# Optimization experiments

Hardware: AMD Instinct MI355X
Metric: run time of the kernel (lower is better)

Reference implementation:

```python
import jax, jax.numpy as jnp
import numpy as np

B, C, L = 4, 256, 4096
H = 8
DK = C // H


def setup_inputs() -> dict:
    key = jax.random.key(0)
    kx, kq, kk, kv, kl = jax.random.split(key, 5)
    scale = 1.0 / np.sqrt(C)
    return {
        "x": jax.random.normal(kx, (B, C, L), dtype=jnp.float32),
        "Wq": jax.random.normal(kq, (C, C), dtype=jnp.float32) * scale,
        "Wk": jax.random.normal(kk, (C, C), dtype=jnp.float32) * scale,
        "Wv": jax.random.normal(kv, (C, C), dtype=jnp.float32) * scale,
        "Wl": jax.random.normal(kl, (C, C), dtype=jnp.float32) * scale,
    }


def reference(x, Wq, Wk, Wv, Wl):
    # Conv1d with kernel_size=1, no bias == channel-mixing matmul per position.
    def proj(W, t):  # W: [C_out, C_in], t: [B, C_in, L] -> [B, L, H, DK]
        y = jnp.einsum('oc,bcl->blo', W, t)
        return y.reshape(B, L, H, DK)

    q = proj(Wq, x)  # [B, L, H, DK]
    k = proj(Wk, x)
    v = proj(Wv, x)

    # scores: [B, H, L, L]
    scores = jnp.einsum('bqhd,bkhd->bhqk', q, k) / jnp.sqrt(jnp.float32(DK))
    p_attn = jax.nn.softmax(scores, axis=-1)
    # attention output with post-ReLU: [B, L, H, DK] -> [B, L, C]
    out = jax.nn.relu(jnp.einsum('bhqk,bkhd->bqhd', p_attn, v)).reshape(B, L, C)
    # last_conv: [B, C_out, L]
    return jnp.einsum('oc,blc->bol', Wl, out)
```

## Files before the change

kernel.cpp:

```cpp
#include <hip/hip_runtime.h>

#define L_DIM 4096
#define C_DIM 256
#define B_DIM 4
#define NH 8
#define DK 32

#define QSCALE 0.25507694f

typedef __bf16 bf16x8 __attribute__((ext_vector_type(8)));
typedef float  f32x4  __attribute__((ext_vector_type(4)));
typedef float  f32x8  __attribute__((ext_vector_type(8)));
typedef float  f32x16 __attribute__((ext_vector_type(16)));

static __device__ __forceinline__ unsigned pk_bf16(float lo, float hi) {
    unsigned a = __builtin_bit_cast(unsigned, lo) + 0x8000u;
    unsigned b = __builtin_bit_cast(unsigned, hi) + 0x8000u;
    return __builtin_amdgcn_perm(b, a, 0x07060302u);
}

__global__ __launch_bounds__(256) void transpose_x_kernel(
    const float* __restrict__ x, __bf16* __restrict__ xt)
{
    const int t  = threadIdx.x;
    const int l0 = blockIdx.x * 64;
    const int c0 = blockIdx.y * 64;
    const int b  = blockIdx.z;

    __shared__ __attribute__((aligned(16))) float T[64][65];

    {
        const int r  = t >> 2;
        const int lc = (t & 3) * 16;
        const float* xp = x + ((size_t)b * C_DIM + c0 + r) * L_DIM + l0 + lc;
        #pragma unroll
        for (int k = 0; k < 4; ++k)
            *(f32x4*)&T[r][lc + k * 4] = *(const f32x4*)(xp + k * 4);
    }
    __syncthreads();
    {
        const int l  = t >> 2;
        const int cc = (t & 3) * 16;
        unsigned u[8];
        #pragma unroll
        for (int i = 0; i < 8; ++i)
            u[i] = pk_bf16(T[cc + 2 * i][l], T[cc + 2 * i + 1][l]);
        __bf16* op = xt + ((size_t)b * L_DIM + l0 + l) * C_DIM + c0 + cc;
        *(uint4*)op       = make_uint4(u[0], u[1], u[2], u[3]);
        *(uint4*)(op + 8) = make_uint4(u[4], u[5], u[6], u[7]);
    }
}

__global__ __launch_bounds__(256) void proj_mfma_kernel(
    const __bf16* __restrict__ xt, const float* __restrict__ Wq,
    const float* __restrict__ Wk, const float* __restrict__ Wv,
    __bf16* __restrict__ Qb, __bf16* __restrict__ Kb, __bf16* __restrict__ Vb)
{
    const int t    = threadIdx.x;
    const int wave = t >> 6;
    const int lane = t & 63;
    const int n32  = lane & 31;
    const int hl   = lane >> 5;
    const int l0   = blockIdx.x * 128;
    const int ob   = blockIdx.y & 1;
    const int p    = blockIdx.y >> 1;
    const int b    = blockIdx.z;
    const float* W = (p == 0) ? Wq : ((p == 1) ? Wk : Wv);
    const float sc = (p == 0) ? QSCALE : 1.0f;

    __shared__ __attribute__((aligned(16))) __bf16 Wt[128][72];
    __shared__ __attribute__((aligned(16))) __bf16 Xs[128][72];

    const int wo  = t >> 1, wcc = (t & 1) * 32;
    const int xl  = t >> 1, xcc = (t & 1) * 32;
    const float*  wg = W + (size_t)(ob * 128 + wo) * C_DIM + wcc;
    const __bf16* xg = xt + ((size_t)b * L_DIM + l0 + xl) * C_DIM + xcc;

    const int moff = (wave & 1) * 64;
    const int noff = (wave >> 1) * 64;

    f32x16 acc[2][2];
    #pragma unroll
    for (int i = 0; i < 2; ++i)
        #pragma unroll
        for (int j = 0; j < 2; ++j)
            #pragma unroll
            for (int r = 0; r < 16; ++r) acc[i][j][r] = 0.f;

    unsigned wpk[16];
    bf16x8   xpr[4];
    #pragma unroll
    for (int k = 0; k < 8; ++k) {
        f32x4 wv = *(const f32x4*)(wg + k * 4);
        wpk[k * 2]     = pk_bf16(wv[0] * sc, wv[1] * sc);
        wpk[k * 2 + 1] = pk_bf16(wv[2] * sc, wv[3] * sc);
    }
    #pragma unroll
    for (int g = 0; g < 4; ++g) xpr[g] = *(const bf16x8*)(xg + g * 8);

    for (int bk = 0; bk < 4; ++bk) {
        __syncthreads();
        #pragma unroll
        for (int g = 0; g < 4; ++g) {
            *(uint4*)&Wt[wo][wcc + g * 8] =
                make_uint4(wpk[g*4], wpk[g*4+1], wpk[g*4+2], wpk[g*4+3]);
            *(bf16x8*)&Xs[xl][xcc + g * 8] = xpr[g];
        }
        if (bk < 3) {
            #pragma unroll
            for (int k = 0; k < 8; ++k) {
                f32x4 wv = *(const f32x4*)(wg + (bk + 1) * 64 + k * 4);
                wpk[k * 2]     = pk_bf16(wv[0] * sc, wv[1] * sc);
                wpk[k * 2 + 1] = pk_bf16(wv[2] * sc, wv[3] * sc);
            }
            #pragma unroll
            for (int g = 0; g < 4; ++g)
                xpr[g] = *(const bf16x8*)(xg + (bk + 1) * 64 + g * 8);
        }
        __syncthreads();

        #pragma unroll
        for (int ks = 0; ks < 4; ++ks) {
            bf16x8 a0 = *(const bf16x8*)&Wt[moff + n32     ][ks * 16 + hl * 8];
            bf16x8 a1 = *(const bf16x8*)&Wt[moff + 32 + n32][ks * 16 + hl * 8];
            bf16x8 b0 = *(const bf16x8*)&Xs[noff + n32     ][ks * 16 + hl * 8];
            bf16x8 b1 = *(const bf16x8*)&Xs[noff + 32 + n32][ks * 16 + hl * 8];
            acc[0][0] = __builtin_amdgcn_mfma_f32_32x32x16_bf16(a0, b0, acc[0][0], 0, 0, 0);
            acc[0][1] = __builtin_amdgcn_mfma_f32_32x32x16_bf16(a0, b1, acc[0][1], 0, 0, 0);
            acc[1][0] = __builtin_amdgcn_mfma_f32_32x32x16_bf16(a1, b0, acc[1][0], 0, 0, 0);
            acc[1][1] = __builtin_amdgcn_mfma_f32_32x32x16_bf16(a1, b1, acc[1][1], 0, 0, 0);
        }
    }

    #pragma unroll
    for (int mt = 0; mt < 2; ++mt) {
        const int o32 = ob * 128 + moff + mt * 32;
        const int h   = o32 >> 5;
        const int bh  = b * NH + h;
        #pragma unroll
        for (int nt = 0; nt < 2; ++nt) {
            const int l = l0 + noff + nt * 32 + n32;
            if (p < 2) {
                __bf16* out = ((p == 0) ? Qb : Kb) + ((size_t)bh * L_DIM + l) * DK;
                #pragma unroll
                for (int g = 0; g < 4; ++g) {
                    unsigned u0 = pk_bf16(acc[mt][nt][g*4],     acc[mt][nt][g*4+1]);
                    unsigned u1 = pk_bf16(acc[mt][nt][g*4+2],   acc[mt][nt][g*4+3]);
                    *(uint2*)(out + 4 * hl + 8 * g) = make_uint2(u0, u1);
                }
            } else {
                #pragma unroll
                for (int r = 0; r < 16; ++r) {
                    const int dk = (r & 3) + 4 * hl + 8 * (r >> 2);
                    Vb[((size_t)bh * DK + dk) * L_DIM + l] = (__bf16)acc[mt][nt][r];
                }
            }
        }
    }
}

__global__ __launch_bounds__(256) void attn_kernel(
    const __bf16* __restrict__ Q, const __bf16* __restrict__ K,
    const __bf16* __restrict__ V, __bf16* __restrict__ Op0,
    __bf16* __restrict__ Op1, float* __restrict__ Ls)
{
    const int tid   = threadIdx.x;
    const int lane  = tid & 63;
    const int n32   = lane & 31;
    const int hl    = lane >> 5;
    const int wave  = tid >> 6;
    const int h     = blockIdx.y;
    const int b     = blockIdx.z >> 1;
    const int khalf = blockIdx.z & 1;
    const int bh    = b * NH + h;
    const int q0    = blockIdx.x * 256 + wave * 64;

    __shared__ __attribute__((aligned(16))) __bf16 Ks[2][128][40];
    __shared__ __attribute__((aligned(16))) __bf16 Vs[2][32][136];

    bf16x8 qf[2][2];
    #pragma unroll
    for (int qt = 0; qt < 2; ++qt) {
        const __bf16* qp = Q + ((size_t)bh * L_DIM + q0 + qt * 32 + n32) * DK;
        qf[qt][0] = *(const bf16x8*)(qp + hl * 8);
        qf[qt][1] = *(const bf16x8*)(qp + 16 + hl * 8);
    }

    f32x16 oacc[2], lacc[2];
    #pragma unroll
    for (int qt = 0; qt < 2; ++qt)
        #pragma unroll
        for (int r = 0; r < 16; ++r) { oacc[qt][r] = 0.f; lacc[qt][r] = 0.f; }

    const f32x16 z16 = {};

    bf16x8 ones;
    #pragma unroll
    for (int j = 0; j < 8; ++j) ones[j] = (__bf16)1.0f;

    const __bf16* kg = K + (size_t)bh * L_DIM * DK + (size_t)khalf * 2048 * DK
                         + (tid >> 1) * DK + (tid & 1) * 16;
    const __bf16* vg = V + ((size_t)bh * DK + (tid >> 3)) * L_DIM
                         + khalf * 2048 + (tid & 7) * 16;
    const int kr = tid >> 1, kc = (tid & 1) * 16;
    const int j16 = (tid & 7) * 16;
    const int vr  = tid >> 3;

    bf16x8 kreg0 = *(const bf16x8*)(kg);
    bf16x8 kreg1 = *(const bf16x8*)(kg + 8);
    bf16x8 vreg0 = *(const bf16x8*)(vg);
    bf16x8 vreg1 = *(const bf16x8*)(vg + 8);
    {
        *(bf16x8*)&Ks[0][kr][kc]     = kreg0;
        *(bf16x8*)&Ks[0][kr][kc + 8] = kreg1;
        union { bf16x8 v; uint2 u2[2]; } v0, v1;
        v0.v = vreg0; v1.v = vreg1;
        *(uint2*)&Vs[0][vr][j16]      = v0.u2[0];
        *(uint2*)&Vs[0][vr][j16 + 8]  = v0.u2[1];
        *(uint2*)&Vs[0][vr][j16 + 4]  = v1.u2[0];
        *(uint2*)&Vs[0][vr][j16 + 12] = v1.u2[1];
    }
    kreg0 = *(const bf16x8*)(kg + (size_t)1 * 128 * DK);
    kreg1 = *(const bf16x8*)(kg + (size_t)1 * 128 * DK + 8);
    vreg0 = *(const bf16x8*)(vg + 128);
    vreg1 = *(const bf16x8*)(vg + 128 + 8);

    #pragma unroll 2
    for (int kt = 0; kt < 16; ++kt) {
        const int cur = kt & 1;
        __syncthreads();

        if (kt < 15) {
            *(bf16x8*)&Ks[cur ^ 1][kr][kc]     = kreg0;
            *(bf16x8*)&Ks[cur ^ 1][kr][kc + 8] = kreg1;
            union { bf16x8 v; uint2 u2[2]; } v0, v1;
            v0.v = vreg0; v1.v = vreg1;
            *(uint2*)&Vs[cur ^ 1][vr][j16]      = v0.u2[0];
            *(uint2*)&Vs[cur ^ 1][vr][j16 + 8]  = v0.u2[1];
            *(uint2*)&Vs[cur ^ 1][vr][j16 + 4]  = v1.u2[0];
            *(uint2*)&Vs[cur ^ 1][vr][j16 + 12] = v1.u2[1];
            const int nkt = (kt + 2) & 15;
            kreg0 = *(const bf16x8*)(kg + (size_t)nkt * 128 * DK);
            kreg1 = *(const bf16x8*)(kg + (size_t)nkt * 128 * DK + 8);
            vreg0 = *(const bf16x8*)(vg + nkt * 128);
            vreg1 = *(const bf16x8*)(vg + nkt * 128 + 8);
        }

        __builtin_amdgcn_s_setprio(1);
        #pragma unroll
        for (int mt = 0; mt < 4; ++mt) {
            bf16x8 kf0 = *(const bf16x8*)&Ks[cur][mt * 32 + n32][hl * 8];
            bf16x8 kf1 = *(const bf16x8*)&Ks[cur][mt * 32 + n32][16 + hl * 8];
            bf16x8 vfA = *(const bf16x8*)&Vs[cur][n32][mt * 32 + hl * 8];
            bf16x8 vfB = *(const bf16x8*)&Vs[cur][n32][mt * 32 + 16 + hl * 8];
            #pragma unroll
            for (int qt = 0; qt < 2; ++qt) {
                f32x16 s = __builtin_amdgcn_mfma_f32_32x32x16_bf16(
                    kf0, qf[qt][0], z16, 0, 0, 0);
                s = __builtin_amdgcn_mfma_f32_32x32x16_bf16(
                    kf1, qf[qt][1], s, 0, 0, 0);

                f32x8 e0, e1;
                #pragma unroll
                for (int r = 0; r < 8; ++r) {
                    e0[r] = __builtin_amdgcn_exp2f(s[r]);
                    e1[r] = __builtin_amdgcn_exp2f(s[8 + r]);
                }
                bf16x8 p0 = __builtin_convertvector(e0, bf16x8);
                bf16x8 p1 = __builtin_convertvector(e1, bf16x8);

                oacc[qt] = __builtin_amdgcn_mfma_f32_32x32x16_bf16(
                    vfA,  p0, oacc[qt], 0, 0, 0);
                lacc[qt] = __builtin_amdgcn_mfma_f32_32x32x16_bf16(
                    ones, p0, lacc[qt], 0, 0, 0);
                oacc[qt] = __builtin_amdgcn_mfma_f32_32x32x16_bf16(
                    vfB,  p1, oacc[qt], 0, 0, 0);
                lacc[qt] = __builtin_amdgcn_mfma_f32_32x32x16_bf16(
                    ones, p1, lacc[qt], 0, 0, 0);
            }
        }
        __builtin_amdgcn_s_setprio(0);
    }

    __bf16* Op = khalf ? Op1 : Op0;
    #pragma unroll
    for (int qt = 0; qt < 2; ++qt) {
        const int l = q0 + qt * 32 + n32;
        __bf16* ap = Op + ((size_t)b * L_DIM + l) * C_DIM + h * 32 + 4 * hl;
        #pragma unroll
        for (int g = 0; g < 4; ++g) {
            *(uint2*)(ap + 8 * g) = make_uint2(
                pk_bf16(oacc[qt][g*4],     oacc[qt][g*4+1]),
                pk_bf16(oacc[qt][g*4+2],   oacc[qt][g*4+3]));
        }
        Ls[((size_t)khalf * B_DIM * NH + bh) * L_DIM + l] = lacc[qt][0];
    }
}

__global__ __launch_bounds__(256) void final_mfma_kernel(
    const __bf16* __restrict__ Op0, const __bf16* __restrict__ Op1,
    const float* __restrict__ Ls, const float* __restrict__ Wl,
    float* __restrict__ y)
{
    const int t    = threadIdx.x;
    const int wave = t >> 6;
    const int lane = t & 63;
    const int n32  = lane & 31;
    const int hl   = lane >> 5;
    const int l0   = blockIdx.x * 64;
    const int ob   = blockIdx.y;
    const int b    = blockIdx.z;

    __shared__ __attribute__((aligned(16))) __bf16 Wt[128][72];
    __shared__ __attribute__((aligned(16))) __bf16 Xs[64][72];

    const int wo  = t >> 1, wcc = (t & 1) * 32;
    const int xl  = t >> 2, xcc = (t & 3) * 16;
    const float* wg = Wl + (size_t)(ob * 128 + wo) * C_DIM + wcc;
    const size_t obase = ((size_t)b * L_DIM + l0 + xl) * C_DIM + xcc;

    float inv[4];
    {
        const int lidx = l0 + xl;
        #pragma unroll
        for (int bk = 0; bk < 4; ++bk) {
            const int hh = (bk * 64 + xcc) >> 5;
            const float l1 = Ls[((size_t)0 * B_DIM * NH + b * NH + hh) * L_DIM + lidx];
            const float l2 = Ls[((size_t)1 * B_DIM * NH + b * NH + hh) * L_DIM + lidx];
            inv[bk] = __builtin_amdgcn_rcpf(l1 + l2);
        }
    }

    const int moff = (wave & 1) * 64;
    const int noff = (wave >> 1) * 32;

    f32x16 acc[2];
    #pragma unroll
    for (int i = 0; i < 2; ++i)
        #pragma unroll
        for (int r = 0; r < 16; ++r) acc[i][r] = 0.f;

    unsigned wpk[16];
    bf16x8   o1r, o2r;
    #pragma unroll
    for (int k = 0; k < 8; ++k) {
        f32x4 wv = *(const f32x4*)(wg + k * 4);
        wpk[k * 2]     = pk_bf16(wv[0], wv[1]);
        wpk[k * 2 + 1] = pk_bf16(wv[2], wv[3]);
    }
    o1r = *(const bf16x8*)(Op0 + obase);
    o2r = *(const bf16x8*)(Op1 + obase);
    bf16x8 o1r2 = *(const bf16x8*)(Op0 + obase + 8);
    bf16x8 o2r2 = *(const bf16x8*)(Op1 + obase + 8);

    for (int bk = 0; bk < 4; ++bk) {
        __syncthreads();
        #pragma unroll
        for (int g = 0; g < 4; ++g)
            *(uint4*)&Wt[wo][wcc + g * 8] =
                make_uint4(wpk[g*4], wpk[g*4+1], wpk[g*4+2], wpk[g*4+3]);
        {
            unsigned u[4];
            #pragma unroll
            for (int i = 0; i < 4; ++i) {
                float v0 = ((float)o1r[2*i]   + (float)o2r[2*i]  ) * inv[bk];
                float v1 = ((float)o1r[2*i+1] + (float)o2r[2*i+1]) * inv[bk];
                v0 = v0 > 0.f ? v0 : 0.f;
                v1 = v1 > 0.f ? v1 : 0.f;
                u[i] = pk_bf16(v0, v1);
            }
            *(uint4*)&Xs[xl][xcc] = make_uint4(u[0], u[1], u[2], u[3]);
            #pragma unroll
            for (int i = 0; i < 4; ++i) {
                float v0 = ((float)o1r2[2*i]   + (float)o2r2[2*i]  ) * inv[bk];
                float v1 = ((float)o1r2[2*i+1] + (float)o2r2[2*i+1]) * inv[bk];
                v0 = v0 > 0.f ? v0 : 0.f;
                v1 = v1 > 0.f ? v1 : 0.f;
                u[i] = pk_bf16(v0, v1);
            }
            *(uint4*)&Xs[xl][xcc + 8] = make_uint4(u[0], u[1], u[2], u[3]);
        }
        if (bk < 3) {
            #pragma unroll
            for (int k = 0; k < 8; ++k) {
                f32x4 wv = *(const f32x4*)(wg + (bk + 1) * 64 + k * 4);
                wpk[k * 2]     = pk_bf16(wv[0], wv[1]);
                wpk[k * 2 + 1] = pk_bf16(wv[2], wv[3]);
            }
            o1r  = *(const bf16x8*)(Op0 + obase + (bk + 1) * 64);
            o2r  = *(const bf16x8*)(Op1 + obase + (bk + 1) * 64);
            o1r2 = *(const bf16x8*)(Op0 + obase + (bk + 1) * 64 + 8);
            o2r2 = *(const bf16x8*)(Op1 + obase + (bk + 1) * 64 + 8);
        }
        __syncthreads();

        #pragma unroll
        for (int ks = 0; ks < 4; ++ks) {
            bf16x8 a0 = *(const bf16x8*)&Wt[moff + n32     ][ks * 16 + hl * 8];
            bf16x8 a1 = *(const bf16x8*)&Wt[moff + 32 + n32][ks * 16 + hl * 8];
            bf16x8 b0 = *(const bf16x8*)&Xs[noff + n32     ][ks * 16 + hl * 8];
            acc[0] = __builtin_amdgcn_mfma_f32_32x32x16_bf16(a0, b0, acc[0], 0, 0, 0);
            acc[1] = __builtin_amdgcn_mfma_f32_32x32x16_bf16(a1, b0, acc[1], 0, 0, 0);
        }
    }

    #pragma unroll
    for (int mt = 0; mt < 2; ++mt) {
        #pragma unroll
        for (int r = 0; r < 16; ++r) {
            const int o = ob * 128 + moff + mt * 32 + (r & 3) + 4 * hl + 8 * (r >> 2);
            y[((size_t)b * C_DIM + o) * L_DIM + l0 + noff + n32] = acc[mt][r];
        }
    }
}

extern "C" void kernel_launch(void* const* d_in, const int* in_sizes, int n_in,
                              void* d_out, int out_size, void* d_ws, size_t ws_size,
                              hipStream_t stream)
{
    const float* x  = (const float*)d_in[0];
    const float* Wq = (const float*)d_in[1];
    const float* Wk = (const float*)d_in[2];
    const float* Wv = (const float*)d_in[3];
    const float* Wl = (const float*)d_in[4];
    float* y = (float*)d_out;

    const size_t n = (size_t)B_DIM * NH * L_DIM * DK;
    __bf16* Qb  = (__bf16*)d_ws;
    __bf16* Kb  = Qb + n;
    __bf16* Vb  = Kb + n;
    __bf16* Xt  = Vb + n;
    __bf16* Op0 = Xt;
    __bf16* Op1 = Xt + n;
    float*  Ls  = (float*)(Op1 + n);

    transpose_x_kernel<<<dim3(L_DIM/64, C_DIM/64, B_DIM), 256, 0, stream>>>(x, Xt);
    proj_mfma_kernel<<<dim3(L_DIM/128, 6, B_DIM), 256, 0, stream>>>(
        Xt, Wq, Wk, Wv, Qb, Kb, Vb);
    attn_kernel<<<dim3(L_DIM/256, NH, B_DIM * 2), 256, 0, stream>>>(
        Qb, Kb, Vb, Op0, Op1, Ls);
    final_mfma_kernel<<<dim3(L_DIM/64, 2, B_DIM), 256, 0, stream>>>(
        Op0, Op1, Ls, Wl, y);
}
```

Baseline: 211.2 us.

## Replace ones-MFMA row sums with VALU sums and split K/V tile processing

The softmax denominator used to be accumulated with extra MFMAs against a ones vector. It is now summed on the VALU from the fp32 exponentials, with one cross-half shuffle at the end. That removes a third of the MFMA work in the attention inner loop and frees the lacc accumulator registers. The loop is also restructured so the first half of the K/V fragments is read and computed before the next tile's shared-memory stores and global prefetch are issued, overlapping them with compute. The sum now uses fp32 exponentials instead of bf16-rounded ones, which changes numerics slightly.

```diff
diff --git a/kernel.cpp b/kernel.cpp
--- a/kernel.cpp
+++ b/kernel.cpp
@@ -159,6 +159,31 @@
     }
 }
 
+#define SCORE_TILE(K0, K1, V0, V1)                                            \
+    _Pragma("unroll")                                                         \
+    for (int qt = 0; qt < 2; ++qt) {                                          \
+        f32x16 s = __builtin_amdgcn_mfma_f32_32x32x16_bf16(                   \
+            K0, qf[qt][0], z16, 0, 0, 0);                                     \
+        s = __builtin_amdgcn_mfma_f32_32x32x16_bf16(K1, qf[qt][1], s, 0, 0, 0); \
+        f32x8 e0, e1;                                                         \
+        _Pragma("unroll")                                                     \
+        for (int r = 0; r < 8; ++r) {                                         \
+            e0[r] = __builtin_amdgcn_exp2f(s[r]);                             \
+            e1[r] = __builtin_amdgcn_exp2f(s[8 + r]);                         \
+        }                                                                     \
+        bf16x8 p0 = __builtin_convertvector(e0, bf16x8);                      \
+        bf16x8 p1 = __builtin_convertvector(e1, bf16x8);                      \
+        oacc[qt] = __builtin_amdgcn_mfma_f32_32x32x16_bf16(                   \
+            V0, p0, oacc[qt], 0, 0, 0);                                       \
+        oacc[qt] = __builtin_amdgcn_mfma_f32_32x32x16_bf16(                   \
+            V1, p1, oacc[qt], 0, 0, 0);                                       \
+        f32x8 es = e0 + e1;                                                   \
+        f32x4 es4;                                                            \
+        _Pragma("unroll")                                                     \
+        for (int r = 0; r < 4; ++r) es4[r] = es[r] + es[r + 4];               \
+        lsum[qt] += (es4[0] + es4[1]) + (es4[2] + es4[3]);                    \
+    }
+
 __global__ __launch_bounds__(256) void attn_kernel(
     const __bf16* __restrict__ Q, const __bf16* __restrict__ K,
     const __bf16* __restrict__ V, __bf16* __restrict__ Op0,
@@ -186,17 +211,14 @@
         qf[qt][1] = *(const bf16x8*)(qp + 16 + hl * 8);
     }
 
-    f32x16 oacc[2], lacc[2];
+    f32x16 oacc[2];
+    float  lsum[2] = {0.f, 0.f};
     #pragma unroll
     for (int qt = 0; qt < 2; ++qt)
         #pragma unroll
-        for (int r = 0; r < 16; ++r) { oacc[qt][r] = 0.f; lacc[qt][r] = 0.f; }
+        for (int r = 0; r < 16; ++r) oacc[qt][r] = 0.f;
 
     const f32x16 z16 = {};
-
-    bf16x8 ones;
-    #pragma unroll
-    for (int j = 0; j < 8; ++j) ones[j] = (__bf16)1.0f;
 
     const __bf16* kg = K + (size_t)bh * L_DIM * DK + (size_t)khalf * 2048 * DK
                          + (tid >> 1) * DK + (tid & 1) * 16;
@@ -229,6 +251,29 @@
     for (int kt = 0; kt < 16; ++kt) {
         const int cur = kt & 1;
         __syncthreads();
+
+        bf16x8 kA0 = *(const bf16x8*)&Ks[cur][n32     ][hl * 8];
+        bf16x8 kA1 = *(const bf16x8*)&Ks[cur][n32     ][16 + hl * 8];
+        bf16x8 kB0 = *(const bf16x8*)&Ks[cur][32 + n32][hl * 8];
+        bf16x8 kB1 = *(const bf16x8*)&Ks[cur][32 + n32][16 + hl * 8];
+        bf16x8 vA0 = *(const bf16x8*)&Vs[cur][n32][     hl * 8];
+        bf16x8 vA1 = *(const bf16x8*)&Vs[cur][n32][16 + hl * 8];
+        bf16x8 vB0 = *(const bf16x8*)&Vs[cur][n32][32 + hl * 8];
+        bf16x8 vB1 = *(const bf16x8*)&Vs[cur][n32][48 + hl * 8];
+
+        __builtin_amdgcn_s_setprio(1);
+        SCORE_TILE(kA0, kA1, vA0, vA1)
+        SCORE_TILE(kB0, kB1, vB0, vB1)
+        __builtin_amdgcn_s_setprio(0);
+
+        kA0 = *(const bf16x8*)&Ks[cur][64 + n32][hl * 8];
+        kA1 = *(const bf16x8*)&Ks[cur][64 + n32][16 + hl * 8];
+        kB0 = *(const bf16x8*)&Ks[cur][96 + n32][hl * 8];
+        kB1 = *(const bf16x8*)&Ks[cur][96 + n32][16 + hl * 8];
+        vA0 = *(const bf16x8*)&Vs[cur][n32][64 + hl * 8];
+        vA1 = *(const bf16x8*)&Vs[cur][n32][80 + hl * 8];
+        vB0 = *(const bf16x8*)&Vs[cur][n32][96 + hl * 8];
+        vB1 = *(const bf16x8*)&Vs[cur][n32][112 + hl * 8];
 
         if (kt < 15) {
             *(bf16x8*)&Ks[cur ^ 1][kr][kc]     = kreg0;
@@ -247,44 +292,15 @@
         }
 
         __builtin_amdgcn_s_setprio(1);
-        #pragma unroll
-        for (int mt = 0; mt < 4; ++mt) {
-            bf16x8 kf0 = *(const bf16x8*)&Ks[cur][mt * 32 + n32][hl * 8];
-            bf16x8 kf1 = *(const bf16x8*)&Ks[cur][mt * 32 + n32][16 + hl * 8];
-            bf16x8 vfA = *(const bf16x8*)&Vs[cur][n32][mt * 32 + hl * 8];
-            bf16x8 vfB = *(const bf16x8*)&Vs[cur][n32][mt * 32 + 16 + hl * 8];
-            #pragma unroll
-            for (int qt = 0; qt < 2; ++qt) {
-                f32x16 s = __builtin_amdgcn_mfma_f32_32x32x16_bf16(
-                    kf0, qf[qt][0], z16, 0, 0, 0);
-                s = __builtin_amdgcn_mfma_f32_32x32x16_bf16(
-                    kf1, qf[qt][1], s, 0, 0, 0);
-
-                f32x8 e0, e1;
-                #pragma unroll
-                for (int r = 0; r < 8; ++r) {
-                    e0[r] = __builtin_amdgcn_exp2f(s[r]);
-                    e1[r] = __builtin_amdgcn_exp2f(s[8 + r]);
-                }
-                bf16x8 p0 = __builtin_convertvector(e0, bf16x8);
-                bf16x8 p1 = __builtin_convertvector(e1, bf16x8);
-
-                oacc[qt] = __builtin_amdgcn_mfma_f32_32x32x16_bf16(
-                    vfA,  p0, oacc[qt], 0, 0, 0);
-                lacc[qt] = __builtin_amdgcn_mfma_f32_32x32x16_bf16(
-                    ones, p0, lacc[qt], 0, 0, 0);
-                oacc[qt] = __builtin_amdgcn_mfma_f32_32x32x16_bf16(
-                    vfB,  p1, oacc[qt], 0, 0, 0);
-                lacc[qt] = __builtin_amdgcn_mfma_f32_32x32x16_bf16(
-                    ones, p1, lacc[qt], 0, 0, 0);
-            }
-        }
+        SCORE_TILE(kA0, kA1, vA0, vA1)
+        SCORE_TILE(kB0, kB1, vB0, vB1)
         __builtin_amdgcn_s_setprio(0);
     }
 
     __bf16* Op = khalf ? Op1 : Op0;
     #pragma unroll
     for (int qt = 0; qt < 2; ++qt) {
+        const float tot = lsum[qt] + __shfl_xor(lsum[qt], 32);
         const int l = q0 + qt * 32 + n32;
         __bf16* ap = Op + ((size_t)b * L_DIM + l) * C_DIM + h * 32 + 4 * hl;
         #pragma unroll
@@ -293,7 +309,7 @@
                 pk_bf16(oacc[qt][g*4],     oacc[qt][g*4+1]),
                 pk_bf16(oacc[qt][g*4+2],   oacc[qt][g*4+3]));
         }
-        Ls[((size_t)khalf * B_DIM * NH + bh) * L_DIM + l] = lacc[qt][0];
+        Ls[((size_t)khalf * B_DIM * NH + bh) * L_DIM + l] = tot;
     }
 }
 
```

New measurement: 224.3 us. 6.2% more time.
